# Performance work log

Measured on AMD Instinct MI355X. Metric: run time of the kernel, lower is better.

## Reference

```python
import jax, jax.numpy as jnp
import numpy as np

NUM_HEADS = 8


def _mab(Q, K, Wq, bq, Wk, bk, Wv, bv, Wo, bo):
    # MAB with ln=False, dropout=0 (eval). Scale is sqrt(dim_V), matching source.
    B, Lq, _ = Q.shape
    Lk = K.shape[1]
    Dv = Wq.shape[1]
    dh = Dv // NUM_HEADS
    q = (Q @ Wq + bq).reshape(B, Lq, NUM_HEADS, dh).transpose(0, 2, 1, 3)
    k = (K @ Wk + bk).reshape(B, Lk, NUM_HEADS, dh).transpose(0, 2, 1, 3)
    v = (K @ Wv + bv).reshape(B, Lk, NUM_HEADS, dh).transpose(0, 2, 1, 3)
    A = jax.nn.softmax(jnp.einsum('bhqd,bhkd->bhqk', q, k) / jnp.sqrt(jnp.float32(Dv)), axis=-1)
    O = (q + jnp.einsum('bhqk,bhkd->bhqd', A, v)).transpose(0, 2, 1, 3).reshape(B, Lq, Dv)
    return O + jax.nn.relu(O @ Wo + bo)


def _forward(x, adj, gin_W, gin_b, geW1, geb1, geW2, geb2,
             gnW1, gnb1, gnW2, gnb2, goW, gob, S,
             mWq, mbq, mWk, mbk, mWv, mbv, mWo, mbo, finW, finb):
    B, V, T, D = x.shape
    Hd = gin_W.shape[1]
    # --- GNN encoder (adj path) ---
    h = x.reshape(B, V, T * D) @ gin_W + gin_b            # [B,V,H]
    # edge_mlp first linear on cat([h_i,h_j]) == h@Wi (row) + h@Wj (col); avoids 2H concat
    Wi, Wj = geW1[:Hd], geW1[Hd:]
    pre = (h @ Wi)[:, :, None, :] + (h @ Wj)[:, None, :, :] + geb1   # [B,V,V,H]
    e = jax.nn.relu(jax.nn.relu(pre) @ geW2 + geb2)       # [B,V,V,H]
    agg = jnp.einsum('bijh,bij->bih', e, adj)             # mask * sum over j, fused
    node = jax.nn.relu(jax.nn.relu(agg @ gnW1 + gnb1) @ gnW2 + gnb2)
    enc = node @ goW + gob                                # [B,V,H]
    # --- decoder: PMA + SAB + SAB + Linear ---
    o = _mab(jnp.broadcast_to(S, (B,) + S.shape[1:]), enc,
             mWq[0], mbq[0], mWk[0], mbk[0], mWv[0], mbv[0], mWo[0], mbo[0])
    o = _mab(o, o, mWq[1], mbq[1], mWk[1], mbk[1], mWv[1], mbv[1], mWo[1], mbo[1])
    o = _mab(o, o, mWq[2], mbq[2], mWk[2], mbk[2], mWv[2], mbv[2], mWo[2], mbo[2])
    out = o @ finW + finb                                 # [B,num_slots,T*OD]
    return out.reshape(B, S.shape[1], T, finW.shape[1] // T)


def setup_inputs() -> dict:
    key = jax.random.key(0)
    ks = jax.random.split(key, 16)
    B, V, T, D = 4, 256, 12, 4
    H, NS, OD = 256, 16, 32

    def w(k, shape, s=0.02):
        return s * jax.random.normal(k, shape, jnp.float32)

    return {
        'x': jax.random.normal(ks[0], (B, V, T, D), jnp.float32),
        'adj': (jax.random.uniform(ks[1], (B, V, V)) > 0.5).astype(jnp.float32),
        'gin_W': w(ks[2], (T * D, H)), 'gin_b': jnp.zeros((H,), jnp.float32),
        'geW1': w(ks[3], (2 * H, H)), 'geb1': jnp.zeros((H,), jnp.float32),
        'geW2': w(ks[4], (H, H)), 'geb2': jnp.zeros((H,), jnp.float32),
        'gnW1': w(ks[5], (H, H)), 'gnb1': jnp.zeros((H,), jnp.float32),
        'gnW2': w(ks[6], (H, H)), 'gnb2': jnp.zeros((H,), jnp.float32),
        'goW': w(ks[7], (H, H)), 'gob': jnp.zeros((H,), jnp.float32),
        'S': w(ks[8], (1, NS, H), 0.05),
        'mWq': w(ks[9], (3, H, H)), 'mbq': jnp.zeros((3, H), jnp.float32),
        'mWk': w(ks[10], (3, H, H)), 'mbk': jnp.zeros((3, H), jnp.float32),
        'mWv': w(ks[11], (3, H, H)), 'mbv': jnp.zeros((3, H), jnp.float32),
        'mWo': w(ks[12], (3, H, H)), 'mbo': jnp.zeros((3, H), jnp.float32),
        'finW': w(ks[13], (H, T * OD)), 'finb': jnp.zeros((T * OD,), jnp.float32),
    }


def reference(x, adj, gin_W, gin_b, geW1, geb1, geW2, geb2,
              gnW1, gnb1, gnW2, gnb2, goW, gob, S,
              mWq, mbq, mWk, mbk, mWv, mbv, mWo, mbo, finW, finb):
    return _forward(x, adj, gin_W, gin_b, geW1, geb1, geW2, geb2,
                    gnW1, gnb1, gnW2, gnb2, goW, gob, S,
                    mWq, mbq, mWk, mbk, mWv, mbv, mWo, mbo, finW, finb)
```

## Files before the change

### kernel.cpp

```cpp
#include <hip/hip_runtime.h>
#include <hip/hip_bf16.h>

typedef unsigned short u16;
typedef __bf16 bf8v __attribute__((ext_vector_type(8)));
typedef float f4v __attribute__((ext_vector_type(4)));

__device__ __forceinline__ float b2f(u16 v) {
  union { unsigned u; float f; } x; x.u = ((unsigned)v) << 16; return x.f;
}
__device__ __forceinline__ u16 f2b(float f) {
  union { float f; unsigned u; } x; x.f = f;
  unsigned r = (x.u + 0x7FFFu + ((x.u >> 16) & 1u)) >> 16;
  return (u16)r;
}
__device__ __forceinline__ unsigned pkbf(float a, float b) {
  union { __hip_bfloat162 h; unsigned u; } c;
  c.h = __float22bfloat162_rn(make_float2(a, b));
  return c.u;
}
__device__ __forceinline__ void up2(unsigned u, float& lo, float& hi) {
  union { unsigned x; float f; } a, b;
  a.x = u << 16; b.x = u & 0xffff0000u; lo = a.f; hi = b.f;
}

#define NFRAG 19
struct PreArgs {
  const float* fsrc[NFRAG];
  u16* fdst[NFRAG];
  int fstride[NFRAG];
  int fbase[NFRAG + 1];
  int fragTiles, hBase, prepBid, q1Bid;
  const float *x, *ginW, *ginb;
  u16* h_bf;
  const float *mbk, *mbv, *mbq, *S, *mWq;
  float *bkv0, *bqkv1, *bqkv2;
  u16* q1b;
};

__global__ __launch_bounds__(256) void k_pre(PreArgs a) {
  __shared__ u16 ld[256 * 20];
  __shared__ float xs[4][48];
  __shared__ float Ss[4096];
  const int bid = blockIdx.x, t = threadIdx.x;

  if (bid < a.fragTiles) {
    int j = 0;
    while (j + 1 < NFRAG && a.fbase[j + 1] <= bid) j++;
    const int localT = bid - a.fbase[j];
    const float* src = a.fsrc[j];
    const int Ns = a.fstride[j];
    const int n0 = localT * 16;
    {
      const float* s = src + (size_t)t * Ns + n0;
      const float4 v0 = ((const float4*)s)[0], v1 = ((const float4*)s)[1];
      const float4 v2 = ((const float4*)s)[2], v3 = ((const float4*)s)[3];
      unsigned* row = (unsigned*)(ld + t * 20);
      row[0] = pkbf(v0.x, v0.y); row[1] = pkbf(v0.z, v0.w);
      row[2] = pkbf(v1.x, v1.y); row[3] = pkbf(v1.z, v1.w);
      row[4] = pkbf(v2.x, v2.y); row[5] = pkbf(v2.z, v2.w);
      row[6] = pkbf(v3.x, v3.y); row[7] = pkbf(v3.z, v3.w);
    }
    __syncthreads();
    u16* dst = a.fdst[j] + (size_t)localT * 4096;
#pragma unroll
    for (int s2 = 0; s2 < 2; s2++) {
      const int o = t * 2 + s2, kt = o >> 6, lane = o & 63;
      const int nlo = lane & 15, bk = kt * 32 + ((lane >> 4) << 3);
      union { u16 h[8]; uint4 q; } pk;
#pragma unroll
      for (int j2 = 0; j2 < 8; j2++) pk.h[j2] = ld[(bk + j2) * 20 + nlo];
      *(uint4*)(dst + (size_t)(kt * 64 + lane) * 8) = pk.q;
    }
    return;
  }
  if (bid >= a.hBase && bid < a.hBase + 256) {
    const int row0 = (bid - a.hBase) * 4;
    if (t < 192) {
      const int rr = t / 48, k = t % 48;
      xs[rr][k] = a.x[(size_t)(row0 + rr) * 48 + k];
    }
    __syncthreads();
    const float bias = a.ginb[t];
    float acc[4] = {bias, bias, bias, bias};
    for (int k = 0; k < 48; k++) {
      const float w = a.ginW[(size_t)k * 256 + t];
#pragma unroll
      for (int rr = 0; rr < 4; rr++) acc[rr] += xs[rr][k] * w;
    }
#pragma unroll
    for (int rr = 0; rr < 4; rr++) a.h_bf[(size_t)(row0 + rr) * 256 + t] = f2b(acc[rr]);
    return;
  }
  if (bid == a.prepBid) {
    a.bkv0[t] = a.mbk[t]; a.bkv0[256 + t] = a.mbv[t];
    a.bqkv1[t] = a.mbq[256 + t]; a.bqkv1[256 + t] = a.mbk[256 + t]; a.bqkv1[512 + t] = a.mbv[256 + t];
    a.bqkv2[t] = a.mbq[512 + t]; a.bqkv2[256 + t] = a.mbk[512 + t]; a.bqkv2[512 + t] = a.mbv[512 + t];
    return;
  }
  if (bid == a.q1Bid) {
    for (int idx = t; idx < 4096; idx += 256) Ss[idx] = a.S[idx];
    __syncthreads();
    float acc[16];
#pragma unroll
    for (int r = 0; r < 16; r++) acc[r] = 0.f;
    for (int k = 0; k < 256; k++) {
      const float w = a.mWq[(size_t)k * 256 + t];
#pragma unroll
      for (int r = 0; r < 16; r++) acc[r] += Ss[r * 256 + k] * w;
    }
    const float bq = a.mbq[t];
#pragma unroll
    for (int r = 0; r < 16; r++) a.q1b[r * 256 + t] = f2b(acc[r] + bq);
    return;
  }
}

__global__ __launch_bounds__(256) void k_wiwj(
    const u16* __restrict__ h, const u16* __restrict__ frag,
    float* __restrict__ hWiF, u16* __restrict__ hWjB) {
  __shared__ __align__(16) u16 As[64 * 264];
  const int t = threadIdx.x, lane = t & 63, wv = t >> 6;
  const int m0 = blockIdx.x * 64, n0 = blockIdx.y * 128;
  {
    const int row = t >> 2, ch = t & 3;
#pragma unroll
    for (int s = 0; s < 8; s++)
      *(uint4*)(As + row * 264 + ch * 64 + s * 8) =
          *(const uint4*)(h + (size_t)(m0 + row) * 256 + ch * 64 + s * 8);
  }
  __syncthreads();
  f4v acc[4][2];
#pragma unroll
  for (int mt = 0; mt < 4; mt++)
#pragma unroll
    for (int nt = 0; nt < 2; nt++) acc[mt][nt] = (f4v){0.f, 0.f, 0.f, 0.f};
  const int Tw = (n0 >> 4) + wv * 2;
#pragma unroll
  for (int kt = 0; kt < 8; kt++) {
    bf8v af[4], bf[2];
#pragma unroll
    for (int mt = 0; mt < 4; mt++)
      af[mt] = *(const bf8v*)(As + (mt * 16 + (lane & 15)) * 264 + kt * 32 + ((lane >> 4) << 3));
#pragma unroll
    for (int nt = 0; nt < 2; nt++)
      bf[nt] = *(const bf8v*)(frag + ((size_t)((Tw + nt) * 8 + kt) * 64 + lane) * 8);
#pragma unroll
    for (int mt = 0; mt < 4; mt++)
#pragma unroll
      for (int nt = 0; nt < 2; nt++)
        acc[mt][nt] = __builtin_amdgcn_mfma_f32_16x16x32_bf16(af[mt], bf[nt], acc[mt][nt], 0, 0, 0);
  }
#pragma unroll
  for (int mt = 0; mt < 4; mt++)
#pragma unroll
    for (int nt = 0; nt < 2; nt++) {
      const int n = n0 + wv * 32 + nt * 16 + (lane & 15);
      const int mb = m0 + mt * 16 + ((lane >> 4) << 2);
#pragma unroll
      for (int r = 0; r < 4; r++) {
        if (n < 256)
          hWiF[(size_t)(mb + r) * 256 + n] = acc[mt][nt][r];
        else
          hWjB[(size_t)(mb + r) * 256 + (n - 256)] = f2b(acc[mt][nt][r]);
      }
    }
}

__global__ __launch_bounds__(256, 2) void k_edge(
    const float* __restrict__ hWiF, const u16* __restrict__ hWjB,
    const float* __restrict__ adj, const float* __restrict__ geb1,
    const u16* __restrict__ fragW2, const float* __restrict__ geb2,
    u16* __restrict__ aggB) {
  __shared__ __align__(16) u16 As[64 * 280];
  __shared__ float hi[256];
  __shared__ int jlist[256];
  __shared__ int cnt;
  const int t = threadIdx.x, lane = t & 63, wv = t >> 6;
  const int b = blockIdx.x >> 8, i = blockIdx.x & 255;
  if (t == 0) cnt = 0;
  __syncthreads();
  {
    const float a = adj[(size_t)(b * 256 + i) * 256 + t];
    hi[t] = hWiF[(size_t)(b * 256 + i) * 256 + t] + geb1[t];
    if (a != 0.f) { const int p = atomicAdd(&cnt, 1); jlist[p] = t; }
  }
  __syncthreads();
  const int nact = cnt;
  if (nact == 0) {
    if (lane < 16) {
#pragma unroll
      for (int nt = 0; nt < 4; nt++)
        aggB[(size_t)(b * 256 + i) * 256 + wv * 64 + nt * 16 + lane] = 0;
    }
    return;
  }
  const int nch = (nact + 63) >> 6;
  float bias2[4];
#pragma unroll
  for (int nt = 0; nt < 4; nt++) bias2[nt] = geb2[wv * 64 + nt * 16 + (lane & 15)];
  float aggAcc[4] = {0.f, 0.f, 0.f, 0.f};
  const u16* fw = fragW2 + lane * 8;

  for (int c = 0; c < nch; c++) {
    const int rows = min(64, nact - c * 64);
    {
      const int r = t >> 2, q = t & 3;
      const bool valid = (r < rows);
      const int j = valid ? jlist[c * 64 + r] : jlist[0];
      const uint4* s4 = (const uint4*)(hWjB + (size_t)(b * 256 + j) * 256 + q * 64);
      u16* dstrow = As + r * 280 + q * 72;
#pragma unroll
      for (int ii = 0; ii < 8; ii++) {
        const uint4 v = s4[ii];
        const int k = q * 64 + ii * 8;
        float f0, f1, f2, f3, f4, f5, f6, f7;
        up2(v.x, f0, f1); up2(v.y, f2, f3); up2(v.z, f4, f5); up2(v.w, f6, f7);
        uint4 qd;
        qd.x = pkbf(fmaxf(f0 + hi[k + 0], 0.f), fmaxf(f1 + hi[k + 1], 0.f));
        qd.y = pkbf(fmaxf(f2 + hi[k + 2], 0.f), fmaxf(f3 + hi[k + 3], 0.f));
        qd.z = pkbf(fmaxf(f4 + hi[k + 4], 0.f), fmaxf(f5 + hi[k + 5], 0.f));
        qd.w = pkbf(fmaxf(f6 + hi[k + 6], 0.f), fmaxf(f7 + hi[k + 7], 0.f));
        *(uint4*)(dstrow + ii * 8) = qd;
      }
    }
    __syncthreads();
    f4v acc[4][4];
#pragma unroll
    for (int jt = 0; jt < 4; jt++)
#pragma unroll
      for (int nt = 0; nt < 4; nt++) acc[jt][nt] = (f4v){0.f, 0.f, 0.f, 0.f};
    bf8v bcur[4];
#pragma unroll
    for (int nt = 0; nt < 4; nt++)
      bcur[nt] = *(const bf8v*)(fw + (size_t)((wv * 4 + nt) * 8 + 0) * 512);
#pragma unroll
    for (int kt = 0; kt < 8; kt++) {
      bf8v bnxt[4];
      if (kt < 7) {
#pragma unroll
        for (int nt = 0; nt < 4; nt++)
          bnxt[nt] = *(const bf8v*)(fw + (size_t)((wv * 4 + nt) * 8 + kt + 1) * 512);
      }
      bf8v af[4];
      const int coff = (kt >> 1) * 72 + (kt & 1) * 32 + ((lane >> 4) << 3);
#pragma unroll
      for (int jt = 0; jt < 4; jt++)
        af[jt] = *(const bf8v*)(As + (jt * 16 + (lane & 15)) * 280 + coff);
#pragma unroll
      for (int nt = 0; nt < 4; nt++)
#pragma unroll
        for (int jt = 0; jt < 4; jt++)
          acc[jt][nt] = __builtin_amdgcn_mfma_f32_16x16x32_bf16(af[jt], bcur[nt], acc[jt][nt], 0, 0, 0);
      if (kt < 7) {
#pragma unroll
        for (int nt = 0; nt < 4; nt++) bcur[nt] = bnxt[nt];
      }
    }
    const int rbase = (lane >> 4) * 4;
#pragma unroll
    for (int nt = 0; nt < 4; nt++) {
      float s = 0.f;
#pragma unroll
      for (int jt = 0; jt < 4; jt++) {
        const int r0 = jt * 16 + rbase;
#pragma unroll
        for (int r = 0; r < 4; r++) {
          const float e = fmaxf(acc[jt][nt][r] + bias2[nt], 0.f);
          s += (r0 + r < rows) ? e : 0.f;
        }
      }
      s += __shfl_xor(s, 16);
      s += __shfl_xor(s, 32);
      aggAcc[nt] += s;
    }
    __syncthreads();
  }
  if (lane < 16) {
#pragma unroll
    for (int nt = 0; nt < 4; nt++) {
      const int n = wv * 64 + nt * 16 + lane;
      aggB[(size_t)(b * 256 + i) * 256 + n] = f2b(aggAcc[nt]);
    }
  }
}

#define NBLK 32

__device__ void g32(const u16* Al, const u16* frag, const float* bias, int relu,
                    u16* Ol, int t) {
  const int lane = t & 63, wv = t >> 6;
  f4v acc[2][4];
#pragma unroll
  for (int mt = 0; mt < 2; mt++)
#pragma unroll
    for (int nt = 0; nt < 4; nt++) acc[mt][nt] = (f4v){0.f, 0.f, 0.f, 0.f};
#pragma unroll
  for (int kt = 0; kt < 8; kt++) {
    bf8v af[2], bf[4];
#pragma unroll
    for (int mt = 0; mt < 2; mt++)
      af[mt] = *(const bf8v*)(Al + (mt * 16 + (lane & 15)) * 264 + kt * 32 + ((lane >> 4) << 3));
#pragma unroll
    for (int nt = 0; nt < 4; nt++)
      bf[nt] = *(const bf8v*)(frag + ((size_t)((wv * 4 + nt) * 8 + kt) * 64 + lane) * 8);
#pragma unroll
    for (int mt = 0; mt < 2; mt++)
#pragma unroll
      for (int nt = 0; nt < 4; nt++)
        acc[mt][nt] = __builtin_amdgcn_mfma_f32_16x16x32_bf16(af[mt], bf[nt], acc[mt][nt], 0, 0, 0);
  }
#pragma unroll
  for (int mt = 0; mt < 2; mt++)
#pragma unroll
    for (int nt = 0; nt < 4; nt++) {
      const int col = wv * 64 + nt * 16 + (lane & 15);
      const float bv = bias[col];
#pragma unroll
      for (int r = 0; r < 4; r++) {
        const int row = mt * 16 + ((lane >> 4) << 2) + r;
        float v = acc[mt][nt][r] + bv;
        if (relu) v = fmaxf(v, 0.f);
        Ol[row * 264 + col] = f2b(v);
      }
    }
}

__device__ void g32kv(const u16* Al, const u16* frag, const float* bias,
                      u16* outG, int t) {
  const int lane = t & 63, wv = t >> 6;
  f4v acc[2][8];
#pragma unroll
  for (int mt = 0; mt < 2; mt++)
#pragma unroll
    for (int nt = 0; nt < 8; nt++) acc[mt][nt] = (f4v){0.f, 0.f, 0.f, 0.f};
#pragma unroll
  for (int kt = 0; kt < 8; kt++) {
    bf8v af[2];
#pragma unroll
    for (int mt = 0; mt < 2; mt++)
// ... 48 lines not shown
      up2(k4.w, kv[c4 * 8 + 6], kv[c4 * 8 + 7]);
    }
    for (int r = 0; r < 16; r++) {
      float s = 0.f;
#pragma unroll
      for (int d = 0; d < 32; d++) s += qs[r * 32 + d] * kv[d];
      sc[r * 256 + t] = s * 0.0625f;
    }
  }
  __syncthreads();
  for (int r = wv * 4; r < wv * 4 + 4; r++) {
    float v[4];
    float mx = -1e30f;
#pragma unroll
    for (int q2 = 0; q2 < 4; q2++) {
      v[q2] = sc[r * 256 + lane + q2 * 64];
      mx = fmaxf(mx, v[q2]);
    }
    for (int off = 32; off; off >>= 1) mx = fmaxf(mx, __shfl_xor(mx, off));
    float sum = 0.f;
#pragma unroll
    for (int q2 = 0; q2 < 4; q2++) { v[q2] = __expf(v[q2] - mx); sum += v[q2]; }
    for (int off = 32; off; off >>= 1) sum += __shfl_xor(sum, off);
    const float inv = 1.f / sum;
#pragma unroll
    for (int q2 = 0; q2 < 4; q2++) sc[r * 256 + lane + q2 * 64] = v[q2] * inv;
  }
  __syncthreads();
  for (int u = t; u < 1024; u += 256) {
    const int row = u >> 2, part = u & 3;
    const uint4 v4 = *(const uint4*)(vbuf + (size_t)(b * Lk + row) * 512 + hd * 32 + part * 8);
    float f0, f1, f2, f3, f4, f5, f6, f7;
    up2(v4.x, f0, f1); up2(v4.y, f2, f3); up2(v4.z, f4, f5); up2(v4.w, f6, f7);
    float4* d = (float4*)(vs + row * 32 + part * 8);
    d[0] = make_float4(f0, f1, f2, f3);
    d[1] = make_float4(f4, f5, f6, f7);
  }
  __syncthreads();
  const int r0 = t >> 5, d = t & 31;
  float a0 = qs[r0 * 32 + d], a1 = qs[(r0 + 8) * 32 + d];
#pragma unroll 4
  for (int j = 0; j < Lk; j++) {
    const float vv = vs[j * 32 + d];
    a0 += sc[r0 * 256 + j] * vv;
    a1 += sc[(r0 + 8) * 256 + j] * vv;
  }
  const int c0 = hd * 32 + d;
  oF[(size_t)(b * 16 + r0) * 256 + c0] = a0;
  oB[(size_t)(b * 16 + r0) * 256 + c0] = f2b(a0);
  oF[(size_t)(b * 16 + r0 + 8) * 256 + c0] = a1;
  oB[(size_t)(b * 16 + r0 + 8) * 256 + c0] = f2b(a1);
}


template <int NT>
__device__ __forceinline__ void wprojGn(
    const u16* __restrict__ o1b, const float* __restrict__ o1f,
    const u16* __restrict__ frag, const float* __restrict__ bias,
    u16* actL, float* residL, int b, int T0, int lane) {
  f4v acc[NT];
#pragma unroll
  for (int nt = 0; nt < NT; nt++) acc[nt] = (f4v){0.f, 0.f, 0.f, 0.f};
  const u16* abase = o1b + (size_t)(b * 16 + (lane & 15)) * 256 + ((lane >> 4) << 3);
#pragma unroll
  for (int kt = 0; kt < 8; kt++) {
    const bf8v af = *(const bf8v*)(abase + kt * 32);
#pragma unroll
    for (int nt = 0; nt < NT; nt++) {
      const bf8v bf = *(const bf8v*)(frag + ((size_t)((T0 + nt) * 8 + kt) * 64 + lane) * 8);
      acc[nt] = __builtin_amdgcn_mfma_f32_16x16x32_bf16(af, bf, acc[nt], 0, 0, 0);
    }
  }
#pragma unroll
  for (int nt = 0; nt < NT; nt++) {
    const int col = (T0 + nt) * 16 + (lane & 15);
    const float bv = bias[col];
#pragma unroll
    for (int r = 0; r < 4; r++) {
      const int row = ((lane >> 4) << 2) + r;
      const float v = fmaxf(acc[nt][r] + bv, 0.f) + o1f[(size_t)(b * 16 + row) * 256 + col];
      residL[row * 256 + col] = v;
      actL[row * 264 + col] = f2b(v);
    }
  }
}

template <int NT>
__device__ __forceinline__ void wprojQn(
    const u16* actL, const u16* __restrict__ frag,
    const float* __restrict__ bias, u16* qkvL, int T0, int lane) {
  f4v acc[NT];
#pragma unroll
  for (int nt = 0; nt < NT; nt++) acc[nt] = (f4v){0.f, 0.f, 0.f, 0.f};
  const u16* abase = actL + (lane & 15) * 264 + ((lane >> 4) << 3);
#pragma unroll
  for (int kt = 0; kt < 8; kt++) {
    const bf8v af = *(const bf8v*)(abase + kt * 32);
#pragma unroll
    for (int nt = 0; nt < NT; nt++) {
      const bf8v bf = *(const bf8v*)(frag + ((size_t)((T0 + nt) * 8 + kt) * 64 + lane) * 8);
      acc[nt] = __builtin_amdgcn_mfma_f32_16x16x32_bf16(af, bf, acc[nt], 0, 0, 0);
    }
  }
#pragma unroll
  for (int nt = 0; nt < NT; nt++) {
    const int col = (T0 + nt) * 16 + (lane & 15);
    const float bv = bias[col];
// ... 79 lines not shown
      up2(q4.z, qv[c4 * 8 + 4], qv[c4 * 8 + 5]);
      up2(q4.w, qv[c4 * 8 + 6], qv[c4 * 8 + 7]);
    }
  }
  float p[4];
#pragma unroll
  for (int c = 0; c < 4; c++) {
    const int cc = cg * 4 + c;
    const uint4* kp = (const uint4*)(qkvL + cc * 776 + 256 + hd * 32);
    float s = 0.f;
#pragma unroll
    for (int c4 = 0; c4 < 4; c4++) {
      const uint4 k4 = kp[c4];
      float k0, k1;
      up2(k4.x, k0, k1); s += qv[c4 * 8 + 0] * k0 + qv[c4 * 8 + 1] * k1;
      up2(k4.y, k0, k1); s += qv[c4 * 8 + 2] * k0 + qv[c4 * 8 + 3] * k1;
      up2(k4.z, k0, k1); s += qv[c4 * 8 + 4] * k0 + qv[c4 * 8 + 5] * k1;
      up2(k4.w, k0, k1); s += qv[c4 * 8 + 6] * k0 + qv[c4 * 8 + 7] * k1;
    }
    p[c] = s * 0.0625f;
  }
  float mx = fmaxf(fmaxf(p[0], p[1]), fmaxf(p[2], p[3]));
  mx = fmaxf(mx, __shfl_xor(mx, 16));
  mx = fmaxf(mx, __shfl_xor(mx, 32));
  float sum = 0.f;
#pragma unroll
  for (int c = 0; c < 4; c++) { p[c] = __expf(p[c] - mx); sum += p[c]; }
  sum += __shfl_xor(sum, 16);
  sum += __shfl_xor(sum, 32);
  const float inv = 1.f / sum;
#pragma unroll
  for (int c = 0; c < 4; c++) ps[r * 16 + cg * 4 + c] = p[c] * inv;
  float o[8];
#pragma unroll
  for (int j = 0; j < 8; j++) o[j] = qv[cg * 8 + j];
#pragma unroll
  for (int c = 0; c < 16; c++) {
    const float pv = ps[r * 16 + c];
    const uint4 v4 = *(const uint4*)(qkvL + c * 776 + 512 + hd * 32 + cg * 8);
    float v0, v1;
    up2(v4.x, v0, v1); o[0] += pv * v0; o[1] += pv * v1;
    up2(v4.y, v0, v1); o[2] += pv * v0; o[3] += pv * v1;
    up2(v4.z, v0, v1); o[4] += pv * v0; o[5] += pv * v1;
    up2(v4.w, v0, v1); o[6] += pv * v0; o[7] += pv * v1;
  }
  const int col0 = hd * 32 + cg * 8;
#pragma unroll
  for (int j = 0; j < 8; j++) residL[r * 256 + col0 + j] = o[j];
  unsigned* ob = (unsigned*)(actOut + r * 264 + col0);
  ob[0] = pkbf(o[0], o[1]); ob[1] = pkbf(o[2], o[3]);
  ob[2] = pkbf(o[4], o[5]); ob[3] = pkbf(o[6], o[7]);
}

struct TailArgs {
  const u16 *agg, *fGn1, *fGn2, *fGo, *fKV0, *fQKV1, *fQKV2, *fO0, *fO1, *fO2, *fFin, *q1b;
  const float *gnb1, *gnb2, *gob, *bkv0, *bqkv1, *bqkv2, *mbo, *finb;
  u16 *kv1, *o1b;
  float *o1f, *outF;
};

__global__ __launch_bounds__(256) void k_tail1(TailArgs a) {
  __shared__ __align__(16) char smem[33792];
  const int bid = blockIdx.x, t = threadIdx.x;
  u16* actA = (u16*)smem;
  u16* actB = (u16*)(smem + 16896);
  const int r0 = bid * 32;
#pragma unroll
  for (int s = 0; s < 4; s++) {
    const int u = t * 4 + s, row = u >> 5, ch = u & 31;
    *(uint4*)(actA + row * 264 + ch * 8) =
        *(const uint4*)(a.agg + (size_t)(r0 + row) * 256 + ch * 8);
  }
  __syncthreads();
  g32(actA, a.fGn1, a.gnb1, 1, actB, t); __syncthreads();
  g32(actB, a.fGn2, a.gnb2, 1, actA, t); __syncthreads();
  g32(actA, a.fGo, a.gob, 0, actB, t); __syncthreads();
  g32kv(actB, a.fKV0, a.bkv0, a.kv1 + (size_t)r0 * 512, t);
}

__global__ __launch_bounds__(256) void k_tail2(TailArgs a) {
  __shared__ __align__(16) char smem[51200];
  float* qs = (float*)smem;
  float* sc = (float*)(smem + 2048);
  float* vs = (float*)(smem + 18432);
  attn_tile(a.q1b, a.kv1, a.kv1 + 256, a.o1f, a.o1b,
            (int)(blockIdx.x >> 3), (int)(blockIdx.x & 7), qs, sc, vs, (int)threadIdx.x);
}

__global__ __launch_bounds__(512) void k_tail3(TailArgs a) {
  __shared__ __align__(16) char smem[58112];
  const int t = threadIdx.x, lane = t & 63, w = t >> 6;
  const int b = blockIdx.x;
  u16* act0 = (u16*)smem;
  u16* act1 = (u16*)(smem + 8448);
  u16* qkvL = (u16*)(smem + 16896);
  float* residL = (float*)(smem + 41728);
  float* psL = (float*)smem;

  wprojGn<2>(a.o1b, a.o1f, a.fO0, a.mbo, act0, residL, b, w * 2, lane);
  __syncthreads();
  wprojQn<6>(act0, a.fQKV1, a.bqkv1, qkvL, w * 6, lane);
  __syncthreads();
  attnB(qkvL, residL, act1, psL + w * 256, w, lane);
  __syncthreads();
  wprojRn<2>(act1, a.fO1, a.mbo + 256, act0, residL, w * 2, lane);
  __syncthreads();
  wprojQn<6>(act0, a.fQKV2, a.bqkv2, qkvL, w * 6, lane);
  __syncthreads();
  attnB(qkvL, residL, act1, psL + w * 256, w, lane);
  __syncthreads();
  wprojRn<2>(act1, a.fO2, a.mbo + 512, act0, residL, w * 2, lane);
  __syncthreads();
  wprojFn<3>(act0, a.fFin, a.finb, a.outF + (size_t)b * 16 * 384, w * 3, lane);
}

extern "C" void kernel_launch(void* const* d_in, const int* in_sizes, int n_in,
                              void* d_out, int out_size, void* d_ws, size_t ws_size,
                              hipStream_t stream) {
  const float* x    = (const float*)d_in[0];
  const float* adj  = (const float*)d_in[1];
  const float* ginW = (const float*)d_in[2];
  const float* ginb = (const float*)d_in[3];
  const float* geW1 = (const float*)d_in[4];
  const float* geb1 = (const float*)d_in[5];
  const float* geW2 = (const float*)d_in[6];
  const float* geb2 = (const float*)d_in[7];
  const float* gnW1 = (const float*)d_in[8];
  const float* gnb1 = (const float*)d_in[9];
  const float* gnW2 = (const float*)d_in[10];
  const float* gnb2 = (const float*)d_in[11];
  const float* goW  = (const float*)d_in[12];
  const float* gob  = (const float*)d_in[13];
  const float* S    = (const float*)d_in[14];
  const float* mWq  = (const float*)d_in[15];
  const float* mbq  = (const float*)d_in[16];
  const float* mWk  = (const float*)d_in[17];
  const float* mbk  = (const float*)d_in[18];
  const float* mWv  = (const float*)d_in[19];
  const float* mbv  = (const float*)d_in[20];
  const float* mWo  = (const float*)d_in[21];
  const float* mbo  = (const float*)d_in[22];
  const float* finW = (const float*)d_in[23];
  const float* finb = (const float*)d_in[24];
  (void)in_sizes; (void)n_in; (void)out_size; (void)ws_size;

  char* wp = (char*)d_ws;
  size_t off = 0;
  auto alloc = [&](size_t bytes) -> char* {
    char* p = wp + off;
    off += (bytes + 255) & ~(size_t)255;
    return p;
  };
  u16* h_bf     = (u16*)alloc(1024 * 256 * 2);
  float* hWiF   = (float*)alloc((size_t)1024 * 256 * 4);
  u16* hWjB     = (u16*)alloc(1024 * 256 * 2);
  u16* fWiWj    = (u16*)alloc(512 * 256 * 2);
  u16* fW2      = (u16*)alloc(256 * 256 * 2);
  u16* fGn1     = (u16*)alloc(256 * 256 * 2);
  u16* fGn2     = (u16*)alloc(256 * 256 * 2);
  u16* fGo      = (u16*)alloc(256 * 256 * 2);
  u16* fQ0      = (u16*)alloc(256 * 256 * 2);
  u16* fKV0     = (u16*)alloc(512 * 256 * 2);
  u16* fQKV1    = (u16*)alloc(768 * 256 * 2);
  u16* fQKV2    = (u16*)alloc(768 * 256 * 2);
  u16* fO0      = (u16*)alloc(256 * 256 * 2);
  u16* fO1      = (u16*)alloc(256 * 256 * 2);
  u16* fO2      = (u16*)alloc(256 * 256 * 2);
  u16* fFin     = (u16*)alloc(384 * 256 * 2);
  float* bkv0   = (float*)alloc(512 * 4);
  float* bqkv1  = (float*)alloc(768 * 4);
  float* bqkv2  = (float*)alloc(768 * 4);
  u16* q1b      = (u16*)alloc(16 * 256 * 2);
  u16* agg_b    = (u16*)alloc(1024 * 256 * 2);
  u16* kv1      = (u16*)alloc(1024 * 512 * 2);
  float* o1f    = (float*)alloc(64 * 256 * 4);
  u16* o1b      = (u16*)alloc(64 * 256 * 2);

  PreArgs P{};
  int nj = 0, tiles = 0;
  auto addF = [&](const float* s, int stride, u16* d, int nT) {
    P.fsrc[nj] = s; P.fdst[nj] = d; P.fstride[nj] = stride; P.fbase[nj] = tiles;
    tiles += nT; nj++;
  };
  addF(geW1, 256, fWiWj, 16);
  addF(geW1 + 65536, 256, fWiWj + 16 * 4096, 16);
  addF(geW2, 256, fW2, 16);
  addF(gnW1, 256, fGn1, 16);
  addF(gnW2, 256, fGn2, 16);
  addF(goW, 256, fGo, 16);
  addF(mWq, 256, fQ0, 16);
  addF(mWk, 256, fKV0, 16);
  addF(mWv, 256, fKV0 + 16 * 4096, 16);
  addF(mWq + 65536, 256, fQKV1, 16);
  addF(mWk + 65536, 256, fQKV1 + 16 * 4096, 16);
  addF(mWv + 65536, 256, fQKV1 + 32 * 4096, 16);
  addF(mWq + 131072, 256, fQKV2, 16);
  addF(mWk + 131072, 256, fQKV2 + 16 * 4096, 16);
  addF(mWv + 131072, 256, fQKV2 + 32 * 4096, 16);
  addF(mWo, 256, fO0, 16);
  addF(mWo + 65536, 256, fO1, 16);
  addF(mWo + 131072, 256, fO2, 16);
  addF(finW, 384, fFin, 24);
  P.fbase[nj] = tiles;
  P.fragTiles = tiles;
  P.hBase = tiles;
  P.prepBid = tiles + 256;
  P.q1Bid = tiles + 257;
  P.x = x; P.ginW = ginW; P.ginb = ginb; P.h_bf = h_bf;
  P.mbk = mbk; P.mbv = mbv; P.mbq = mbq; P.S = S; P.mWq = mWq;
  P.bkv0 = bkv0; P.bqkv1 = bqkv1; P.bqkv2 = bqkv2; P.q1b = q1b;

  TailArgs T{};
  T.agg = agg_b; T.fGn1 = fGn1; T.fGn2 = fGn2; T.fGo = fGo; T.fKV0 = fKV0;
  T.fQKV1 = fQKV1; T.fQKV2 = fQKV2; T.fO0 = fO0; T.fO1 = fO1; T.fO2 = fO2;
  T.fFin = fFin; T.q1b = q1b;
  T.gnb1 = gnb1; T.gnb2 = gnb2; T.gob = gob;
  T.bkv0 = bkv0; T.bqkv1 = bqkv1; T.bqkv2 = bqkv2; T.mbo = mbo; T.finb = finb;
  T.kv1 = kv1; T.o1b = o1b; T.o1f = o1f; T.outF = (float*)d_out;

  k_pre<<<dim3(tiles + 258), dim3(256), 0, stream>>>(P);
  k_wiwj<<<dim3(16, 4), dim3(256), 0, stream>>>(h_bf, fWiWj, hWiF, hWjB);
  k_edge<<<dim3(1024), dim3(256), 0, stream>>>(hWiF, hWjB, adj, geb1, fW2, geb2, agg_b);
  k_tail1<<<dim3(NBLK), dim3(256), 0, stream>>>(T);
  k_tail2<<<dim3(NBLK), dim3(256), 0, stream>>>(T);
  k_tail3<<<dim3(4), dim3(512), 0, stream>>>(T);
}
```

Before: 248.9 us.

## Fuse all stages into one persistent kernel with software grid barriers

Merges the six separate launches (pre, wiwj, edge, tail1-3) into a single persistent kernel of 512 blocks. The stages are separated by an atomic-counter grid barrier, which is meant to remove launch gaps and per-kernel ramp-up and drain. The tail3 stage is remapped from 512 to 256 threads, so each wave now handles twice the work. The unused fQ0 weight conversion is dropped. The trade-offs are barrier spin cost, a reliance on all 512 blocks being co-resident without any cooperative-launch guarantee, and an extra memset launch.

```diff
diff --git a/kernel.cpp b/kernel.cpp
--- a/kernel.cpp
+++ b/kernel.cpp
@@ -23,8 +23,10 @@
   a.x = u << 16; b.x = u & 0xffff0000u; lo = a.f; hi = b.f;
 }
 
-#define NFRAG 19
-struct PreArgs {
+#define NFRAG 18
+#define GRIDN 512
+
+struct AllArgs {
   const float* fsrc[NFRAG];
   u16* fdst[NFRAG];
   int fstride[NFRAG];
@@ -35,18 +37,41 @@
   const float *mbk, *mbv, *mbq, *S, *mWq;
   float *bkv0, *bqkv1, *bqkv2;
   u16* q1b;
+  const u16* fWiWj;
+  float* hWiF;
+  u16* hWjB;
+  const float *adj, *geb1, *geb2;
+  const u16* fW2;
+  u16* aggB;
+  const u16 *fGn1, *fGn2, *fGo, *fKV0, *fQKV1, *fQKV2, *fO0, *fO1, *fO2, *fFin;
+  const float *gnb1, *gnb2, *gob, *mbo, *finb;
+  u16 *kv1, *o1b;
+  float *o1f, *outF;
+  int* bar;
 };
 
-__global__ __launch_bounds__(256) void k_pre(PreArgs a) {
-  __shared__ u16 ld[256 * 20];
-  __shared__ float xs[4][48];
-  __shared__ float Ss[4096];
-  const int bid = blockIdx.x, t = threadIdx.x;
-
-  if (bid < a.fragTiles) {
+__device__ __forceinline__ void gridbar(int* cnt, int gen) {
+  __syncthreads();
+  if (threadIdx.x == 0) {
+    __threadfence();
+    __hip_atomic_fetch_add(cnt, 1, __ATOMIC_RELAXED, __HIP_MEMORY_SCOPE_AGENT);
+    int it = 0;
+    while (__hip_atomic_load(cnt, __ATOMIC_RELAXED, __HIP_MEMORY_SCOPE_AGENT) < GRIDN * gen) {
+      __builtin_amdgcn_s_sleep(8);
+      if (((++it) & 255) == 0)
+        __hip_atomic_fetch_add(cnt, 0, __ATOMIC_RELAXED, __HIP_MEMORY_SCOPE_AGENT);
+    }
+    __threadfence();
+  }
+  __syncthreads();
+}
+
+__device__ void pre_item(const AllArgs& a, int item, int t, char* smem) {
+  if (item < a.fragTiles) {
+    u16* ld = (u16*)smem;
     int j = 0;
-    while (j + 1 < NFRAG && a.fbase[j + 1] <= bid) j++;
-    const int localT = bid - a.fbase[j];
+    while (j + 1 < NFRAG && a.fbase[j + 1] <= item) j++;
+    const int localT = item - a.fbase[j];
     const float* src = a.fsrc[j];
     const int Ns = a.fstride[j];
     const int n0 = localT * 16;
@@ -73,8 +98,9 @@
     }
     return;
   }
-  if (bid >= a.hBase && bid < a.hBase + 256) {
-    const int row0 = (bid - a.hBase) * 4;
+  if (item < a.prepBid) {
+    float (*xs)[48] = (float (*)[48])(smem + 10240);
+    const int row0 = (item - a.hBase) * 4;
     if (t < 192) {
       const int rr = t / 48, k = t % 48;
       xs[rr][k] = a.x[(size_t)(row0 + rr) * 48 + k];
@@ -91,13 +117,14 @@
     for (int rr = 0; rr < 4; rr++) a.h_bf[(size_t)(row0 + rr) * 256 + t] = f2b(acc[rr]);
     return;
   }
-  if (bid == a.prepBid) {
+  if (item == a.prepBid) {
     a.bkv0[t] = a.mbk[t]; a.bkv0[256 + t] = a.mbv[t];
     a.bqkv1[t] = a.mbq[256 + t]; a.bqkv1[256 + t] = a.mbk[256 + t]; a.bqkv1[512 + t] = a.mbv[256 + t];
     a.bqkv2[t] = a.mbq[512 + t]; a.bqkv2[256 + t] = a.mbk[512 + t]; a.bqkv2[512 + t] = a.mbv[512 + t];
     return;
   }
-  if (bid == a.q1Bid) {
+  if (item == a.q1Bid) {
+    float* Ss = (float*)(smem + 11264);
     for (int idx = t; idx < 4096; idx += 256) Ss[idx] = a.S[idx];
     __syncthreads();
     float acc[16];
@@ -111,22 +138,19 @@
     const float bq = a.mbq[t];
 #pragma unroll
     for (int r = 0; r < 16; r++) a.q1b[r * 256 + t] = f2b(acc[r] + bq);
-    return;
-  }
-}
-
-__global__ __launch_bounds__(256) void k_wiwj(
-    const u16* __restrict__ h, const u16* __restrict__ frag,
-    float* __restrict__ hWiF, u16* __restrict__ hWjB) {
-  __shared__ __align__(16) u16 As[64 * 264];
-  const int t = threadIdx.x, lane = t & 63, wv = t >> 6;
-  const int m0 = blockIdx.x * 64, n0 = blockIdx.y * 128;
+  }
+}
+
+__device__ void wiwj_item(const AllArgs& a, int e, int t, char* smem) {
+  u16* As = (u16*)smem;
+  const int lane = t & 63, wv = t >> 6;
+  const int m0 = (e & 15) * 64, n0 = (e >> 4) * 128;
   {
     const int row = t >> 2, ch = t & 3;
 #pragma unroll
     for (int s = 0; s < 8; s++)
       *(uint4*)(As + row * 264 + ch * 64 + s * 8) =
-          *(const uint4*)(h + (size_t)(m0 + row) * 256 + ch * 64 + s * 8);
+          *(const uint4*)(a.h_bf + (size_t)(m0 + row) * 256 + ch * 64 + s * 8);
   }
   __syncthreads();
   f4v acc[4][2];
@@ -143,7 +167,7 @@
       af[mt] = *(const bf8v*)(As + (mt * 16 + (lane & 15)) * 264 + kt * 32 + ((lane >> 4) << 3));
 #pragma unroll
     for (int nt = 0; nt < 2; nt++)
-      bf[nt] = *(const bf8v*)(frag + ((size_t)((Tw + nt) * 8 + kt) * 64 + lane) * 8);
+      bf[nt] = *(const bf8v*)(a.fWiWj + ((size_t)((Tw + nt) * 8 + kt) * 64 + lane) * 8);
 #pragma unroll
     for (int mt = 0; mt < 4; mt++)
 #pragma unroll
@@ -159,47 +183,43 @@
 #pragma unroll
       for (int r = 0; r < 4; r++) {
         if (n < 256)
-          hWiF[(size_t)(mb + r) * 256 + n] = acc[mt][nt][r];
+          a.hWiF[(size_t)(mb + r) * 256 + n] = acc[mt][nt][r];
         else
-          hWjB[(size_t)(mb + r) * 256 + (n - 256)] = f2b(acc[mt][nt][r]);
+          a.hWjB[(size_t)(mb + r) * 256 + (n - 256)] = f2b(acc[mt][nt][r]);
       }
     }
 }
 
-__global__ __launch_bounds__(256, 2) void k_edge(
-    const float* __restrict__ hWiF, const u16* __restrict__ hWjB,
-    const float* __restrict__ adj, const float* __restrict__ geb1,
-    const u16* __restrict__ fragW2, const float* __restrict__ geb2,
-    u16* __restrict__ aggB) {
-  __shared__ __align__(16) u16 As[64 * 280];
-  __shared__ float hi[256];
-  __shared__ int jlist[256];
-  __shared__ int cnt;
-  const int t = threadIdx.x, lane = t & 63, wv = t >> 6;
-  const int b = blockIdx.x >> 8, i = blockIdx.x & 255;
-  if (t == 0) cnt = 0;
+__device__ void edge_item(const AllArgs& a, int item, int t, char* smem) {
+  u16* As = (u16*)smem;
+  float* hi = (float*)(smem + 35840);
+  int* jlist = (int*)(smem + 36864);
+  int* cnt = (int*)(smem + 37888);
+  const int lane = t & 63, wv = t >> 6;
+  const int b = item >> 8, i = item & 255;
+  if (t == 0) *cnt = 0;
   __syncthreads();
   {
-    const float a = adj[(size_t)(b * 256 + i) * 256 + t];
-    hi[t] = hWiF[(size_t)(b * 256 + i) * 256 + t] + geb1[t];
-    if (a != 0.f) { const int p = atomicAdd(&cnt, 1); jlist[p] = t; }
-  }
-  __syncthreads();
-  const int nact = cnt;
+    const float av = a.adj[(size_t)(b * 256 + i) * 256 + t];
+    hi[t] = a.hWiF[(size_t)(b * 256 + i) * 256 + t] + a.geb1[t];
+    if (av != 0.f) { const int p = atomicAdd(cnt, 1); jlist[p] = t; }
+  }
+  __syncthreads();
+  const int nact = *cnt;
   if (nact == 0) {
     if (lane < 16) {
 #pragma unroll
       for (int nt = 0; nt < 4; nt++)
-        aggB[(size_t)(b * 256 + i) * 256 + wv * 64 + nt * 16 + lane] = 0;
+        a.aggB[(size_t)(b * 256 + i) * 256 + wv * 64 + nt * 16 + lane] = 0;
     }
     return;
   }
   const int nch = (nact + 63) >> 6;
   float bias2[4];
 #pragma unroll
-  for (int nt = 0; nt < 4; nt++) bias2[nt] = geb2[wv * 64 + nt * 16 + (lane & 15)];
+  for (int nt = 0; nt < 4; nt++) bias2[nt] = a.geb2[wv * 64 + nt * 16 + (lane & 15)];
   float aggAcc[4] = {0.f, 0.f, 0.f, 0.f};
-  const u16* fw = fragW2 + lane * 8;
+  const u16* fw = a.fW2 + lane * 8;
 
   for (int c = 0; c < nch; c++) {
     const int rows = min(64, nact - c * 64);
@@ -207,7 +227,7 @@
       const int r = t >> 2, q = t & 3;
       const bool valid = (r < rows);
       const int j = valid ? jlist[c * 64 + r] : jlist[0];
-      const uint4* s4 = (const uint4*)(hWjB + (size_t)(b * 256 + j) * 256 + q * 64);
+      const uint4* s4 = (const uint4*)(a.hWjB + (size_t)(b * 256 + j) * 256 + q * 64);
       u16* dstrow = As + r * 280 + q * 72;
 #pragma unroll
       for (int ii = 0; ii < 8; ii++) {
@@ -279,12 +299,10 @@
 #pragma unroll
     for (int nt = 0; nt < 4; nt++) {
       const int n = wv * 64 + nt * 16 + lane;
-      aggB[(size_t)(b * 256 + i) * 256 + n] = f2b(aggAcc[nt]);
-    }
-  }
-}
-
-#define NBLK 32
+      a.aggB[(size_t)(b * 256 + i) * 256 + n] = f2b(aggAcc[nt]);
+    }
+  }
+}
 
 __device__ void g32(const u16* Al, const u16* frag, const float* bias, int relu,
                     u16* Ol, int t) {
@@ -439,7 +457,6 @@
   oB[(size_t)(b * 16 + r0 + 8) * 256 + c0] = f2b(a1);
 }
 
-
 template <int NT>
 __device__ __forceinline__ void wprojGn(
     const u16* __restrict__ o1b, const float* __restrict__ o1f,
@@ -625,24 +642,15 @@
   ob[2] = pkbf(o[4], o[5]); ob[3] = pkbf(o[6], o[7]);
 }
 
-struct TailArgs {
-  const u16 *agg, *fGn1, *fGn2, *fGo, *fKV0, *fQKV1, *fQKV2, *fO0, *fO1, *fO2, *fFin, *q1b;
-  const float *gnb1, *gnb2, *gob, *bkv0, *bqkv1, *bqkv2, *mbo, *finb;
-  u16 *kv1, *o1b;
-  float *o1f, *outF;
-};
-
-__global__ __launch_bounds__(256) void k_tail1(TailArgs a) {
-  __shared__ __align__(16) char smem[33792];
-  const int bid = blockIdx.x, t = threadIdx.x;
+__device__ void tail1_item(const AllArgs& a, int e, int t, char* smem) {
   u16* actA = (u16*)smem;
   u16* actB = (u16*)(smem + 16896);
-  const int r0 = bid * 32;
+  const int r0 = e * 32;
 #pragma unroll
   for (int s = 0; s < 4; s++) {
     const int u = t * 4 + s, row = u >> 5, ch = u & 31;
     *(uint4*)(actA + row * 264 + ch * 8) =
-        *(const uint4*)(a.agg + (size_t)(r0 + row) * 256 + ch * 8);
+        *(const uint4*)(a.aggB + (size_t)(r0 + row) * 256 + ch * 8);
   }
   __syncthreads();
   g32(actA, a.fGn1, a.gnb1, 1, actB, t); __syncthreads();
@@ -651,40 +659,63 @@
   g32kv(actB, a.fKV0, a.bkv0, a.kv1 + (size_t)r0 * 512, t);
 }
 
-__global__ __launch_bounds__(256) void k_tail2(TailArgs a) {
-  __shared__ __align__(16) char smem[51200];
+__device__ void tail2_item(const AllArgs& a, int e, int t, char* smem) {
   float* qs = (float*)smem;
   float* sc = (float*)(smem + 2048);
   float* vs = (float*)(smem + 18432);
-  attn_tile(a.q1b, a.kv1, a.kv1 + 256, a.o1f, a.o1b,
-            (int)(blockIdx.x >> 3), (int)(blockIdx.x & 7), qs, sc, vs, (int)threadIdx.x);
-}
-
-__global__ __launch_bounds__(512) void k_tail3(TailArgs a) {
-  __shared__ __align__(16) char smem[58112];
-  const int t = threadIdx.x, lane = t & 63, w = t >> 6;
-  const int b = blockIdx.x;
+  attn_tile(a.q1b, a.kv1, a.kv1 + 256, a.o1f, a.o1b, e >> 3, e & 7, qs, sc, vs, t);
+}
+
+__device__ void tail3_item(const AllArgs& a, int b, int t, char* smem) {
+  const int lane = t & 63, w = t >> 6;
   u16* act0 = (u16*)smem;
   u16* act1 = (u16*)(smem + 8448);
   u16* qkvL = (u16*)(smem + 16896);
   float* residL = (float*)(smem + 41728);
   float* psL = (float*)smem;
 
-  wprojGn<2>(a.o1b, a.o1f, a.fO0, a.mbo, act0, residL, b, w * 2, lane);
+  wprojGn<4>(a.o1b, a.o1f, a.fO0, a.mbo, act0, residL, b, w * 4, lane);
   __syncthreads();
   wprojQn<6>(act0, a.fQKV1, a.bqkv1, qkvL, w * 6, lane);
+  wprojQn<6>(act0, a.fQKV1, a.bqkv1, qkvL, 24 + w * 6, lane);
   __syncthreads();
   attnB(qkvL, residL, act1, psL + w * 256, w, lane);
-  __syncthreads();
-  wprojRn<2>(act1, a.fO1, a.mbo + 256, act0, residL, w * 2, lane);
+  attnB(qkvL, residL, act1, psL + w * 256, w + 4, lane);
+  __syncthreads();
+  wprojRn<4>(act1, a.fO1, a.mbo + 256, act0, residL, w * 4, lane);
   __syncthreads();
   wprojQn<6>(act0, a.fQKV2, a.bqkv2, qkvL, w * 6, lane);
+  wprojQn<6>(act0, a.fQKV2, a.bqkv2, qkvL, 24 + w * 6, lane);
   __syncthreads();
   attnB(qkvL, residL, act1, psL + w * 256, w, lane);
-  __syncthreads();
-  wprojRn<2>(act1, a.fO2, a.mbo + 512, act0, residL, w * 2, lane);
-  __syncthreads();
-  wprojFn<3>(act0, a.fFin, a.finb, a.outF + (size_t)b * 16 * 384, w * 3, lane);
+  attnB(qkvL, residL, act1, psL + w * 256, w + 4, lane);
+  __syncthreads();
+  wprojRn<4>(act1, a.fO2, a.mbo + 512, act0, residL, w * 4, lane);
+  __syncthreads();
+  wprojFn<6>(act0, a.fFin, a.finb, a.outF + (size_t)b * 16 * 384, w * 6, lane);
+}
+
+__global__ __launch_bounds__(256, 2) void k_fused(AllArgs a) {
+  __shared__ __align__(16) char smem[58112];
+  const int bid = blockIdx.x, t = threadIdx.x;
+
+  for (int item = bid; item <= a.q1Bid; item += GRIDN) {
+    pre_item(a, item, t, smem);
+    __syncthreads();
+  }
+  gridbar(a.bar, 1);
+  if (bid < 64) wiwj_item(a, bid, t, smem);
+  gridbar(a.bar, 2);
+  for (int item = bid; item < 1024; item += GRIDN) {
+    edge_item(a, item, t, smem);
+    __syncthreads();
+  }
+  gridbar(a.bar, 3);
+  if (bid < 32) tail1_item(a, bid, t, smem);
+  gridbar(a.bar, 4);
+  if (bid < 32) tail2_item(a, bid, t, smem);
+  gridbar(a.bar, 5);
+  if (bid < 4) tail3_item(a, bid, t, smem);
 }
 
 extern "C" void kernel_launch(void* const* d_in, const int* in_sizes, int n_in,
@@ -732,7 +763,6 @@
   u16* fGn1     = (u16*)alloc(256 * 256 * 2);
   u16* fGn2     = (u16*)alloc(256 * 256 * 2);
   u16* fGo      = (u16*)alloc(256 * 256 * 2);
-  u16* fQ0      = (u16*)alloc(256 * 256 * 2);
   u16* fKV0     = (u16*)alloc(512 * 256 * 2);
   u16* fQKV1    = (u16*)alloc(768 * 256 * 2);
   u16* fQKV2    = (u16*)alloc(768 * 256 * 2);
@@ -748,11 +778,12 @@
   u16* kv1      = (u16*)alloc(1024 * 512 * 2);
   float* o1f    = (float*)alloc(64 * 256 * 4);
   u16* o1b      = (u16*)alloc(64 * 256 * 2);
-
-  PreArgs P{};
+  int* bar      = (int*)alloc(256);
+
+  AllArgs A{};
   int nj = 0, tiles = 0;
   auto addF = [&](const float* s, int stride, u16* d, int nT) {
-    P.fsrc[nj] = s; P.fdst[nj] = d; P.fstride[nj] = stride; P.fbase[nj] = tiles;
+    A.fsrc[nj] = s; A.fdst[nj] = d; A.fstride[nj] = stride; A.fbase[nj] = tiles;
     tiles += nT; nj++;
   };
   addF(geW1, 256, fWiWj, 16);
@@ -761,7 +792,6 @@
   addF(gnW1, 256, fGn1, 16);
   addF(gnW2, 256, fGn2, 16);
   addF(goW, 256, fGo, 16);
-  addF(mWq, 256, fQ0, 16);
   addF(mWk, 256, fKV0, 16);
   addF(mWv, 256, fKV0 + 16 * 4096, 16);
   addF(mWq + 65536, 256, fQKV1, 16);
@@ -774,27 +804,23 @@
   addF(mWo + 65536, 256, fO1, 16);
   addF(mWo + 131072, 256, fO2, 16);
   addF(finW, 384, fFin, 24);
-  P.fbase[nj] = tiles;
-  P.fragTiles = tiles;
-  P.hBase = tiles;
-  P.prepBid = tiles + 256;
-  P.q1Bid = tiles + 257;
-  P.x = x; P.ginW = ginW; P.ginb = ginb; P.h_bf = h_bf;
-  P.mbk = mbk; P.mbv = mbv; P.mbq = mbq; P.S = S; P.mWq = mWq;
-  P.bkv0 = bkv0; P.bqkv1 = bqkv1; P.bqkv2 = bqkv2; P.q1b = q1b;
-
-  TailArgs T{};
-  T.agg = agg_b; T.fGn1 = fGn1; T.fGn2 = fGn2; T.fGo = fGo; T.fKV0 = fKV0;
-  T.fQKV1 = fQKV1; T.fQKV2 = fQKV2; T.fO0 = fO0; T.fO1 = fO1; T.fO2 = fO2;
-  T.fFin = fFin; T.q1b = q1b;
-  T.gnb1 = gnb1; T.gnb2 = gnb2; T.gob = gob;
-  T.bkv0 = bkv0; T.bqkv1 = bqkv1; T.bqkv2 = bqkv2; T.mbo = mbo; T.finb = finb;
-  T.kv1 = kv1; T.o1b = o1b; T.o1f = o1f; T.outF = (float*)d_out;
-
-  k_pre<<<dim3(tiles + 258), dim3(256), 0, stream>>>(P);
-  k_wiwj<<<dim3(16, 4), dim3(256), 0, stream>>>(h_bf, fWiWj, hWiF, hWjB);
-  k_edge<<<dim3(1024), dim3(256), 0, stream>>>(hWiF, hWjB, adj, geb1, fW2, geb2, agg_b);
-  k_tail1<<<dim3(NBLK), dim3(256), 0, stream>>>(T);
-  k_tail2<<<dim3(NBLK), dim3(256), 0, stream>>>(T);
-  k_tail3<<<dim3(4), dim3(512), 0, stream>>>(T);
-}
+  A.fbase[nj] = tiles;
+  A.fragTiles = tiles;
+  A.hBase = tiles;
+  A.prepBid = tiles + 256;
+  A.q1Bid = tiles + 257;
+  A.x = x; A.ginW = ginW; A.ginb = ginb; A.h_bf = h_bf;
+  A.mbk = mbk; A.mbv = mbv; A.mbq = mbq; A.S = S; A.mWq = mWq;
+  A.bkv0 = bkv0; A.bqkv1 = bqkv1; A.bqkv2 = bqkv2; A.q1b = q1b;
+  A.fWiWj = fWiWj; A.hWiF = hWiF; A.hWjB = hWjB;
+  A.adj = adj; A.geb1 = geb1; A.geb2 = geb2; A.fW2 = fW2; A.aggB = agg_b;
+  A.fGn1 = fGn1; A.fGn2 = fGn2; A.fGo = fGo; A.fKV0 = fKV0;
+  A.fQKV1 = fQKV1; A.fQKV2 = fQKV2; A.fO0 = fO0; A.fO1 = fO1; A.fO2 = fO2;
+  A.fFin = fFin;
+  A.gnb1 = gnb1; A.gnb2 = gnb2; A.gob = gob; A.mbo = mbo; A.finb = finb;
+  A.kv1 = kv1; A.o1b = o1b; A.o1f = o1f; A.outF = (float*)d_out;
+  A.bar = bar;
+
+  hipMemsetAsync(bar, 0, 256, stream);
+  k_fused<<<dim3(GRIDN), dim3(256), 0, stream>>>(A);
+}
```

New measurement: 492.4 us. 1.98x slower.

## Fuse three tail kernels into one persistent kernel with grid barriers

Applied to the files above, without the earlier changes.

Replaces the three tail launches with a single 32-block kernel that separates the phases with software grid barriers built on an atomic counter, which is reset in the pre kernel. The intent is to remove two kernel launch gaps. The final decoder stage now runs with 256 threads instead of 512, so each wave does twice the work, and the unused fQ0 fragment conversion is dropped. The spin barrier relies on all 32 blocks being co-resident, and the halved thread count may slow the serial tail stage.

```diff
diff --git a/kernel.cpp b/kernel.cpp
--- a/kernel.cpp
+++ b/kernel.cpp
@@ -23,7 +23,9 @@
   a.x = u << 16; b.x = u & 0xffff0000u; lo = a.f; hi = b.f;
 }
 
-#define NFRAG 19
+#define NFRAG 18
+#define NBLK 32
+
 struct PreArgs {
   const float* fsrc[NFRAG];
   u16* fdst[NFRAG];
@@ -35,15 +37,15 @@
   const float *mbk, *mbv, *mbq, *S, *mWq;
   float *bkv0, *bqkv1, *bqkv2;
   u16* q1b;
+  int* bar;
 };
 
 __global__ __launch_bounds__(256) void k_pre(PreArgs a) {
-  __shared__ u16 ld[256 * 20];
-  __shared__ float xs[4][48];
-  __shared__ float Ss[4096];
+  __shared__ __align__(16) char smem[27648];
   const int bid = blockIdx.x, t = threadIdx.x;
 
   if (bid < a.fragTiles) {
+    u16* ld = (u16*)smem;
     int j = 0;
     while (j + 1 < NFRAG && a.fbase[j + 1] <= bid) j++;
     const int localT = bid - a.fbase[j];
@@ -73,7 +75,8 @@
     }
     return;
   }
-  if (bid >= a.hBase && bid < a.hBase + 256) {
+  if (bid < a.prepBid) {
+    float (*xs)[48] = (float (*)[48])(smem + 10240);
     const int row0 = (bid - a.hBase) * 4;
     if (t < 192) {
       const int rr = t / 48, k = t % 48;
@@ -92,12 +95,14 @@
     return;
   }
   if (bid == a.prepBid) {
+    if (t < 64) a.bar[t] = 0;
     a.bkv0[t] = a.mbk[t]; a.bkv0[256 + t] = a.mbv[t];
     a.bqkv1[t] = a.mbq[256 + t]; a.bqkv1[256 + t] = a.mbk[256 + t]; a.bqkv1[512 + t] = a.mbv[256 + t];
     a.bqkv2[t] = a.mbq[512 + t]; a.bqkv2[256 + t] = a.mbk[512 + t]; a.bqkv2[512 + t] = a.mbv[512 + t];
     return;
   }
   if (bid == a.q1Bid) {
+    float* Ss = (float*)(smem + 11264);
     for (int idx = t; idx < 4096; idx += 256) Ss[idx] = a.S[idx];
     __syncthreads();
     float acc[16];
@@ -284,7 +289,21 @@
   }
 }
 
-#define NBLK 32
+__device__ __forceinline__ void gridbar(int* cnt, int gen) {
+  __syncthreads();
+  if (threadIdx.x == 0) {
+    __threadfence();
+    __hip_atomic_fetch_add(cnt, 1, __ATOMIC_RELAXED, __HIP_MEMORY_SCOPE_AGENT);
+    int it = 0;
+    while (__hip_atomic_load(cnt, __ATOMIC_RELAXED, __HIP_MEMORY_SCOPE_AGENT) < NBLK * gen) {
+      __builtin_amdgcn_s_sleep(8);
+      if (((++it) & 255) == 0)
+        __hip_atomic_fetch_add(cnt, 0, __ATOMIC_RELAXED, __HIP_MEMORY_SCOPE_AGENT);
+    }
+    __threadfence();
+  }
+  __syncthreads();
+}
 
 __device__ void g32(const u16* Al, const u16* frag, const float* bias, int relu,
                     u16* Ol, int t) {
@@ -439,7 +458,6 @@
   oB[(size_t)(b * 16 + r0 + 8) * 256 + c0] = f2b(a1);
 }
 
-
 template <int NT>
 __device__ __forceinline__ void wprojGn(
     const u16* __restrict__ o1b, const float* __restrict__ o1f,
@@ -630,14 +648,13 @@
   const float *gnb1, *gnb2, *gob, *bkv0, *bqkv1, *bqkv2, *mbo, *finb;
   u16 *kv1, *o1b;
   float *o1f, *outF;
+  int* bar;
 };
 
-__global__ __launch_bounds__(256) void k_tail1(TailArgs a) {
-  __shared__ __align__(16) char smem[33792];
-  const int bid = blockIdx.x, t = threadIdx.x;
+__device__ void tail1_item(const TailArgs& a, int e, int t, char* smem) {
   u16* actA = (u16*)smem;
   u16* actB = (u16*)(smem + 16896);
-  const int r0 = bid * 32;
+  const int r0 = e * 32;
 #pragma unroll
   for (int s = 0; s < 4; s++) {
     const int u = t * 4 + s, row = u >> 5, ch = u & 31;
@@ -651,40 +668,50 @@
   g32kv(actB, a.fKV0, a.bkv0, a.kv1 + (size_t)r0 * 512, t);
 }
 
-__global__ __launch_bounds__(256) void k_tail2(TailArgs a) {
-  __shared__ __align__(16) char smem[51200];
+__device__ void tail2_item(const TailArgs& a, int e, int t, char* smem) {
   float* qs = (float*)smem;
   float* sc = (float*)(smem + 2048);
   float* vs = (float*)(smem + 18432);
-  attn_tile(a.q1b, a.kv1, a.kv1 + 256, a.o1f, a.o1b,
-            (int)(blockIdx.x >> 3), (int)(blockIdx.x & 7), qs, sc, vs, (int)threadIdx.x);
-}
-
-__global__ __launch_bounds__(512) void k_tail3(TailArgs a) {
-  __shared__ __align__(16) char smem[58112];
-  const int t = threadIdx.x, lane = t & 63, w = t >> 6;
-  const int b = blockIdx.x;
+  attn_tile(a.q1b, a.kv1, a.kv1 + 256, a.o1f, a.o1b, e >> 3, e & 7, qs, sc, vs, t);
+}
+
+__device__ void tail3_item(const TailArgs& a, int b, int t, char* smem) {
+  const int lane = t & 63, w = t >> 6;
   u16* act0 = (u16*)smem;
   u16* act1 = (u16*)(smem + 8448);
   u16* qkvL = (u16*)(smem + 16896);
   float* residL = (float*)(smem + 41728);
   float* psL = (float*)smem;
 
-  wprojGn<2>(a.o1b, a.o1f, a.fO0, a.mbo, act0, residL, b, w * 2, lane);
+  wprojGn<4>(a.o1b, a.o1f, a.fO0, a.mbo, act0, residL, b, w * 4, lane);
   __syncthreads();
   wprojQn<6>(act0, a.fQKV1, a.bqkv1, qkvL, w * 6, lane);
+  wprojQn<6>(act0, a.fQKV1, a.bqkv1, qkvL, 24 + w * 6, lane);
   __syncthreads();
   attnB(qkvL, residL, act1, psL + w * 256, w, lane);
-  __syncthreads();
-  wprojRn<2>(act1, a.fO1, a.mbo + 256, act0, residL, w * 2, lane);
+  attnB(qkvL, residL, act1, psL + w * 256, w + 4, lane);
+  __syncthreads();
+  wprojRn<4>(act1, a.fO1, a.mbo + 256, act0, residL, w * 4, lane);
   __syncthreads();
   wprojQn<6>(act0, a.fQKV2, a.bqkv2, qkvL, w * 6, lane);
+  wprojQn<6>(act0, a.fQKV2, a.bqkv2, qkvL, 24 + w * 6, lane);
   __syncthreads();
   attnB(qkvL, residL, act1, psL + w * 256, w, lane);
-  __syncthreads();
-  wprojRn<2>(act1, a.fO2, a.mbo + 512, act0, residL, w * 2, lane);
-  __syncthreads();
-  wprojFn<3>(act0, a.fFin, a.finb, a.outF + (size_t)b * 16 * 384, w * 3, lane);
+  attnB(qkvL, residL, act1, psL + w * 256, w + 4, lane);
+  __syncthreads();
+  wprojRn<4>(act1, a.fO2, a.mbo + 512, act0, residL, w * 4, lane);
+  __syncthreads();
+  wprojFn<6>(act0, a.fFin, a.finb, a.outF + (size_t)b * 16 * 384, w * 6, lane);
+}
+
+__global__ __launch_bounds__(256) void k_tailF(TailArgs a) {
+  __shared__ __align__(16) char smem[58112];
+  const int bid = blockIdx.x, t = threadIdx.x;
+  tail1_item(a, bid, t, smem);
+  gridbar(a.bar, 1);
+  tail2_item(a, bid, t, smem);
+  gridbar(a.bar, 2);
+  if (bid < 4) tail3_item(a, bid, t, smem);
 }
 
 extern "C" void kernel_launch(void* const* d_in, const int* in_sizes, int n_in,
@@ -732,7 +759,6 @@
   u16* fGn1     = (u16*)alloc(256 * 256 * 2);
   u16* fGn2     = (u16*)alloc(256 * 256 * 2);
   u16* fGo      = (u16*)alloc(256 * 256 * 2);
-  u16* fQ0      = (u16*)alloc(256 * 256 * 2);
   u16* fKV0     = (u16*)alloc(512 * 256 * 2);
   u16* fQKV1    = (u16*)alloc(768 * 256 * 2);
   u16* fQKV2    = (u16*)alloc(768 * 256 * 2);
@@ -748,6 +774,7 @@
   u16* kv1      = (u16*)alloc(1024 * 512 * 2);
   float* o1f    = (float*)alloc(64 * 256 * 4);
   u16* o1b      = (u16*)alloc(64 * 256 * 2);
+  int* bar      = (int*)alloc(256);
 
   PreArgs P{};
   int nj = 0, tiles = 0;
@@ -761,7 +788,6 @@
   addF(gnW1, 256, fGn1, 16);
   addF(gnW2, 256, fGn2, 16);
   addF(goW, 256, fGo, 16);
-  addF(mWq, 256, fQ0, 16);
   addF(mWk, 256, fKV0, 16);
   addF(mWv, 256, fKV0 + 16 * 4096, 16);
   addF(mWq + 65536, 256, fQKV1, 16);
@@ -782,6 +808,7 @@
   P.x = x; P.ginW = ginW; P.ginb = ginb; P.h_bf = h_bf;
   P.mbk = mbk; P.mbv = mbv; P.mbq = mbq; P.S = S; P.mWq = mWq;
   P.bkv0 = bkv0; P.bqkv1 = bqkv1; P.bqkv2 = bqkv2; P.q1b = q1b;
+  P.bar = bar;
 
   TailArgs T{};
   T.agg = agg_b; T.fGn1 = fGn1; T.fGn2 = fGn2; T.fGo = fGo; T.fKV0 = fKV0;
@@ -790,11 +817,10 @@
   T.gnb1 = gnb1; T.gnb2 = gnb2; T.gob = gob;
   T.bkv0 = bkv0; T.bqkv1 = bqkv1; T.bqkv2 = bqkv2; T.mbo = mbo; T.finb = finb;
   T.kv1 = kv1; T.o1b = o1b; T.o1f = o1f; T.outF = (float*)d_out;
+  T.bar = bar;
 
   k_pre<<<dim3(tiles + 258), dim3(256), 0, stream>>>(P);
   k_wiwj<<<dim3(16, 4), dim3(256), 0, stream>>>(h_bf, fWiWj, hWiF, hWjB);
   k_edge<<<dim3(1024), dim3(256), 0, stream>>>(hWiF, hWjB, adj, geb1, fW2, geb2, agg_b);
-  k_tail1<<<dim3(NBLK), dim3(256), 0, stream>>>(T);
-  k_tail2<<<dim3(NBLK), dim3(256), 0, stream>>>(T);
-  k_tail3<<<dim3(4), dim3(512), 0, stream>>>(T);
-}
+  k_tailF<<<dim3(NBLK), dim3(256), 0, stream>>>(T);
+}
```

Result: slower. 287.5 us (+15.5%).
